# Performance work log

Hardware: AMD Instinct MI355X
Metric: run time of the kernel (lower is better)

## Reference

```python
import jax, jax.numpy as jnp
import numpy as np

D, H, T, K = 512, 8, 4, 64   # dim, n_heads, n_tasks, topk_n
HD = D // H
PRUNE, EPS = 1e-3, 1e-8


def _ln(x, g, b, eps=1e-5):
    m = jnp.mean(x, axis=-1, keepdims=True)
    v = jnp.mean((x - m) ** 2, axis=-1, keepdims=True)
    return (x - m) * jax.lax.rsqrt(v + eps) * g + b


def setup_inputs() -> dict:
    key = jax.random.key(0)
    ks = jax.random.split(key, 5)
    B, N = 16, 8192
    tokens = jax.random.normal(ks[0], (B, N, D), jnp.float32)
    key_padding_mask = jax.random.uniform(ks[1], (B, N)) < 0.1  # True marks padding
    q = jax.random.normal(ks[2], (1, T, D), jnp.float32) * 0.02
    in_proj_w = jax.random.normal(ks[3], (3 * D, D), jnp.float32) / np.sqrt(D).astype(np.float32)
    in_proj_b = jnp.zeros((3 * D,), jnp.float32)
    pre_g = jnp.ones((D,), jnp.float32)
    pre_b = jnp.zeros((D,), jnp.float32)
    q_g = jnp.ones((D,), jnp.float32)
    q_b = jnp.zeros((D,), jnp.float32)
    log_tau = jnp.asarray(np.log(0.3), jnp.float32)
    return dict(tokens=tokens, key_padding_mask=key_padding_mask, q=q,
                in_proj_w=in_proj_w, in_proj_b=in_proj_b,
                pre_g=pre_g, pre_b=pre_b, q_g=q_g, q_b=q_b, log_tau=log_tau)


def reference(tokens, key_padding_mask, q, in_proj_w, in_proj_b,
              pre_g, pre_b, q_g, q_b, log_tau):
    B, N, _ = tokens.shape
    kpm = key_padding_mask  # [B,N], True = pad

    normed = _ln(tokens, pre_g, pre_b)                       # [B,N,D]
    tau = jnp.clip(jnp.exp(log_tau), 0.1, 10.0)
    query = _ln(q, q_g, q_b) / tau                           # [1,T,D]

    wq, wk, wv = in_proj_w[:D], in_proj_w[D:2 * D], in_proj_w[2 * D:]
    bq, bk, bv = in_proj_b[:D], in_proj_b[D:2 * D], in_proj_b[2 * D:]

    qp = (query[0] @ wq.T + bq).reshape(T, H, HD)            # [T,H,hd]
    kp = (normed @ wk.T + bk).reshape(B, N, H, HD)           # [B,N,H,hd]

    scores = jnp.einsum('thd,bnhd->bhtn', qp, kp) / np.float32(np.sqrt(HD))
    scores = jnp.where(kpm[:, None, None, :], -jnp.inf, scores)
    attn = jax.nn.softmax(scores, axis=-1)                   # [B,H,T,N]

    alpha = attn.mean(axis=1)                                # [B,T,N]
    alpha = jnp.where(kpm[:, None, :], 0.0, alpha)
    alpha = alpha / jnp.maximum(alpha.sum(-1, keepdims=True), EPS)

    # prune below threshold, with argmax one-hot fallback if everything pruned
    a = jnp.where(alpha < PRUNE, 0.0, alpha)
    a = jnp.where(kpm[:, None, :], 0.0, a)
    s = a.sum(-1, keepdims=True)
    need_fallback = s <= EPS                                 # [B,T,1]
    base = jnp.where(kpm[:, None, :], -1.0, alpha)
    onehot = jax.nn.one_hot(jnp.argmax(base, axis=-1), N, dtype=a.dtype)  # [B,T,N]
    a = jnp.where(need_fallback, onehot, a)
    a = jnp.where(kpm[:, None, :], 0.0, a)
    alpha = a / jnp.maximum(a.sum(-1, keepdims=True), EPS)

    # pool source: tie_mha_v projection of normed inputs
    pool_source = normed @ wv.T + bv                         # [B,N,D]

    # top-k gather + renorm weighting
    topv, topi = jax.lax.top_k(alpha, K)                     # [B,T,K]
    selected = jnp.take_along_axis(pool_source[:, None, :, :], topi[..., None], axis=2)  # [B,T,K,D]
    w = topv / jnp.maximum(topv.sum(-1, keepdims=True), EPS)
    pooled = (w[..., None] * selected).sum(axis=2)           # [B,T,D]
    return pooled
```

## Files before the change

kernel.cpp:

```cpp
#include <hip/hip_runtime.h>
#include <math.h>

#define Dd   512
#define Hh   8
#define Tt   4
#define HDd  64
#define Bb   16
#define Nn   8192
#define HTc  32
#define KS   64
#define NTOK (Bb*Nn)
#define PRUNEc 0.001f
#define EPSc   1e-8f

#define WS_G2     0u
#define WS_C1     65536u
#define WS_C0     65664u
#define WS_M      65792u
#define WS_L      67840u
#define WS_TOPW   69888u
#define WS_TOPI   86272u
#define WS_FLAG   102656u
#define WS_MEAN   131072u
#define WS_INV    655360u
#define WS_MASK8  1179648u
#define WS_SCORES 2097152u

__global__ void tap_detect(const unsigned* mraw, int* flag){
  int tid = threadIdx.x;
  if (tid == 0) *flag = 0;
  __syncthreads();
  int f = 0;
  for (int i = tid; i < NTOK/4; i += 256){
    unsigned v = mraw[i];
    if (v == 0x3f800000u) f |= 2;
    else if (v & ~1u)     f |= 1;
  }
  if (f) atomicOr(flag, f);
}

__global__ void tap_mask(const void* mraw, const int* flag, unsigned char* m8){
  int i = blockIdx.x*256 + threadIdx.x;
  int fl = *flag;
  unsigned char m;
  if (fl & 2)      m = (((const float*)mraw)[i] != 0.0f);
  else if (fl & 1) m = (((const unsigned char*)mraw)[i] != 0);
  else             m = (((const int*)mraw)[i] != 0);
  m8[i] = m;
}

__global__ void tap_prep(const float* q, const float* ipw, const float* ipb,
                         const float* pre_g, const float* pre_b,
                         const float* q_g, const float* q_b, const float* log_tau,
                         float* G2, float* C1, float* C0){
  __shared__ float query[Tt][Dd];
  __shared__ float qps[HDd];
  __shared__ float red[256];
  int tid = threadIdx.x;
  int ht = blockIdx.x;
  int h = ht >> 2, t = ht & 3;
  float tau = expf(log_tau[0]);
  tau = fminf(fmaxf(tau, 0.1f), 10.0f);
  float itau = 1.0f / tau;
  int wv = tid >> 6, lane = tid & 63;
  {
    const float* qr = q + wv*Dd;
    float s = 0.f, ss = 0.f;
    for (int j = lane; j < Dd; j += 64){ float x = qr[j]; s += x; ss += x*x; }
    #pragma unroll
    for (int off = 32; off; off >>= 1){ s += __shfl_down(s, off); ss += __shfl_down(ss, off); }
    s = __shfl(s, 0); ss = __shfl(ss, 0);
    float mean = s * (1.f/Dd);
    float var  = ss * (1.f/Dd) - mean*mean;
    float inv  = rsqrtf(var + 1e-5f);
    for (int j = lane; j < Dd; j += 64){
      float x = qr[j];
      query[wv][j] = ((x - mean)*inv*q_g[j] + q_b[j]) * itau;
    }
  }
  __syncthreads();
  {
    int d = tid >> 2, sub = tid & 3;
    int i = h*HDd + d;
    const float* wrow = ipw + (size_t)i*Dd;
    float acc = 0.f;
    int j0 = sub*128;
    for (int j = 0; j < 128; ++j) acc += query[t][j0+j]*wrow[j0+j];
    red[tid] = acc;
    __syncthreads();
    if (sub == 0) qps[d] = red[tid]+red[tid+1]+red[tid+2]+red[tid+3] + ipb[i];
    __syncthreads();
  }
  float c1p = 0.f, c0p = 0.f;
  for (int jj = 0; jj < 2; ++jj){
    int j = tid + jj*256;
    float acc = 0.f;
    #pragma unroll 8
    for (int d = 0; d < HDd; ++d)
      acc += qps[d] * ipw[(size_t)(Dd + h*HDd + d)*Dd + j];
    float w2 = acc * 0.125f;
    float g2 = w2 * pre_g[j];
    G2[ht*Dd + j] = g2;
    c1p += g2;
    c0p += w2 * pre_b[j];
  }
  if (tid < HDd) c0p += qps[tid] * ipb[Dd + h*HDd + tid] * 0.125f;
  red[tid] = c1p; __syncthreads();
  for (int s = 128; s; s >>= 1){ if (tid < s) red[tid] += red[tid+s]; __syncthreads(); }
  if (tid == 0) C1[ht] = red[0];
  __syncthreads();
  red[tid] = c0p; __syncthreads();
  for (int s = 128; s; s >>= 1){ if (tid < s) red[tid] += red[tid+s]; __syncthreads(); }
  if (tid == 0) C0[ht] = red[0];
}

__global__ __launch_bounds__(256, 3) void tap_scores(
    const float* __restrict__ tokens, const float* __restrict__ G2,
    const float* __restrict__ C1, const float* __restrict__ C0,
    float* __restrict__ scores, float* __restrict__ meanw, float* __restrict__ invw){
  __shared__ float4 xt4[64*33];
  __shared__ float4 g2s4[32*33];
  __shared__ float smean[64], sinv[64];
  int tid = threadIdx.x;
  int tg = tid & 15, hp = tid >> 4;
  int ht0 = hp, ht1 = hp + 16;
  size_t t0 = (size_t)blockIdx.x * 64;
  const float4* tokv = (const float4*)tokens;
  const float4* G2v  = (const float4*)G2;
  int colL = tid & 31, rowBase = tid >> 5;
  float acc[4][2] = {{0.f,0.f},{0.f,0.f},{0.f,0.f},{0.f,0.f}};
  float ps[8] = {0,0,0,0,0,0,0,0}, pss[8] = {0,0,0,0,0,0,0,0};
  for (int c = 0; c < 4; ++c){
    #pragma unroll
    for (int i = 0; i < 8; ++i){
      int row = rowBase + 8*i;
      float4 v = tokv[(t0 + row)*128 + c*32 + colL];
      xt4[row*33 + colL] = v;
      ps[i]  += v.x + v.y + v.z + v.w;
      pss[i] += v.x*v.x + v.y*v.y + v.z*v.z + v.w*v.w;
    }
    #pragma unroll
    for (int i = 0; i < 4; ++i){
      int p = tid + 256*i;
      int row = p >> 5;
      g2s4[row*33 + colL] = G2v[row*128 + c*32 + colL];
    }
    __syncthreads();
    const float4* xb = xt4 + tg*33;
    #pragma unroll 8
    for (int j4 = 0; j4 < 32; ++j4){
      float4 g0 = g2s4[ht0*33 + j4];
      float4 g1 = g2s4[ht1*33 + j4];
      #pragma unroll
      for (int r = 0; r < 4; ++r){
        float4 x = xb[r*528 + j4];
        acc[r][0] += x.x*g0.x + x.y*g0.y + x.z*g0.z + x.w*g0.w;
        acc[r][1] += x.x*g1.x + x.y*g1.y + x.z*g1.z + x.w*g1.w;
      }
    }
    __syncthreads();
  }
  #pragma unroll
  for (int i = 0; i < 8; ++i){
    float s = ps[i], ss = pss[i];
    #pragma unroll
    for (int off = 16; off; off >>= 1){
      s  += __shfl_down(s,  off, 32);
      ss += __shfl_down(ss, off, 32);
    }
    if ((tid & 31) == 0){
      int row = rowBase + 8*i;
      float mean = s * (1.f/512.f);
      float var  = ss * (1.f/512.f) - mean*mean;
      float inv  = rsqrtf(var + 1e-5f);
      smean[row] = mean; sinv[row] = inv;
      meanw[t0 + row] = mean; invw[t0 + row] = inv;
    }
  }
  __syncthreads();
  float c10 = C1[ht0], c11 = C1[ht1], c00 = C0[ht0], c01 = C0[ht1];
  int b  = (int)(t0 >> 13);
  int n0 = (int)(t0 & 8191);
  float* s0p = scores + ((size_t)(b*HTc + ht0))*Nn + n0 + tg;
  float* s1p = scores + ((size_t)(b*HTc + ht1))*Nn + n0 + tg;
  #pragma unroll
  for (int r = 0; r < 4; ++r){
    int row = tg + 16*r;
    float mean = smean[row], inv = sinv[row];
    s0p[16*r] = inv*(acc[r][0] - mean*c10) + c00;
    s1p[16*r] = inv*(acc[r][1] - mean*c11) + c01;
  }
}

__global__ void tap_norm(const float* __restrict__ scores, const unsigned char* __restrict__ m8,
                         float* __restrict__ mrow, float* __restrict__ lrow){
  int R = blockIdx.x;
  int b = R >> 5;
  const float* srow = scores + (size_t)R*Nn;
  const unsigned char* mk = m8 + b*Nn;
  int tid = threadIdx.x;
  int wv = tid >> 6, lane = tid & 63;
  __shared__ float r4[4];
  float v[32];
  float mx = -1e30f;
  #pragma unroll
  for (int i = 0; i < 32; ++i){
    int n = tid + i*256;
    float s = srow[n];
    v[i] = mk[n] ? -1e30f : s;
    mx = fmaxf(mx, v[i]);
  }
  #pragma unroll
  for (int off = 32; off; off >>= 1) mx = fmaxf(mx, __shfl_down(mx, off));
  if (lane == 0) r4[wv] = mx;
  __syncthreads();
  mx = fmaxf(fmaxf(r4[0], r4[1]), fmaxf(r4[2], r4[3]));
  float se = 0.f;
  #pragma unroll
  for (int i = 0; i < 32; ++i) se += expf(v[i] - mx);
  #pragma unroll
  for (int off = 32; off; off >>= 1) se += __shfl_down(se, off);
  __syncthreads();
  if (lane == 0) r4[wv] = se;
  __syncthreads();
  if (tid == 0){ mrow[R] = mx; lrow[R] = r4[0]+r4[1]+r4[2]+r4[3]; }
}

__global__ void tap_alpha(const float* __restrict__ scores, const unsigned char* __restrict__ m8,
                          const float* __restrict__ mrow, const float* __restrict__ lrow,
                          float* __restrict__ topw, int* __restrict__ topi){
  __shared__ float av[Nn];
  __shared__ float lv[1024];
  __shared__ int   li[1024];
  __shared__ float rv[4]; __shared__ int ri[4]; __shared__ int rp[4];
  __shared__ int cnt; __shared__ int sArg;
  int bt = blockIdx.x;
  int b = bt >> 2, t = bt & 3;
  int tid = threadIdx.x;
  int wv = tid >> 6, lane = tid & 63;
  const unsigned char* mk = m8 + b*Nn;
  if (tid == 0) cnt = 0;
  float mh[Hh], il[Hh];
  const float* srows[Hh];
  #pragma unroll
  for (int h = 0; h < Hh; ++h){
    int R = b*HTc + h*Tt + t;
    mh[h] = mrow[R];
    il[h] = 1.0f / lrow[R];
    srows[h] = scores + (size_t)R*Nn;
  }
  float lsum = 0.f;
  float bvv = -2.f; int bii = 1<<30;
  for (int i = 0; i < 32; ++i){
    int n = tid + i*256;
    float a = 0.f;
    if (!mk[n]){
      #pragma unroll
      for (int h = 0; h < Hh; ++h) a += expf(srows[h][n] - mh[h]) * il[h];
      a *= 0.125f;
    }
    av[n] = a;
    lsum += a;
    float bb = mk[n] ? -1.f : a;
    if (bb > bvv || (bb == bvv && n < bii)){ bvv = bb; bii = n; }
  }
  #pragma unroll
  for (int off = 32; off; off >>= 1) lsum += __shfl_down(lsum, off);
  if (lane == 0) rv[wv] = lsum;
  __syncthreads();
  float Sall = rv[0]+rv[1]+rv[2]+rv[3];
  #pragma unroll
  for (int off = 32; off; off >>= 1){
    float ov = __shfl_down(bvv, off);
    int   oi = __shfl_down(bii, off);
    if (ov > bvv || (ov == bvv && oi < bii)){ bvv = ov; bii = oi; }
  }
  __syncthreads();
  if (lane == 0){ rv[wv] = bvv; ri[wv] = bii; }
  __syncthreads();
  if (tid == 0){
    float bv2 = rv[0]; int bi2 = ri[0];
    for (int w2 = 1; w2 < 4; ++w2)
      if (rv[w2] > bv2 || (rv[w2] == bv2 && ri[w2] < bi2)){ bv2 = rv[w2]; bi2 = ri[w2]; }
    sArg = bi2;
  }
  __syncthreads();
  float f1 = 1.0f / fmaxf(Sall, EPSc);
  for (int i = 0; i < 32; ++i){
    int n = tid + i*256;
    float x = av[n] * f1;
    if (x >= PRUNEc){
      int id = atomicAdd(&cnt, 1);
      if (id < 1024){ lv[id] = x; li[id] = n; }
    }
  }
  __syncthreads();
  int L = cnt;
  float* tw = topw + bt*KS;
  int*   ti = topi + bt*KS;
  if (L == 0){
    if (tid < KS){ tw[tid] = (tid == 0) ? 1.f : 0.f; ti[tid] = (tid == 0) ? sArg : 0; }
    return;
  }
  if (L <= KS){
    if (tid < KS){ tw[tid] = (tid < L) ? lv[tid] : 0.f; ti[tid] = (tid < L) ? li[tid] : 0; }
    return;
  }
  for (int k = 0; k < KS; ++k){
    float bv = -1.f; int bn = 1<<30; int bp = -1;
    for (int j = tid; j < L; j += 256){
      float x = lv[j]; int nn = li[j];
      if (x > bv || (x == bv && nn < bn)){ bv = x; bn = nn; bp = j; }
    }
    #pragma unroll
    for (int off = 32; off; off >>= 1){
      float ov = __shfl_down(bv, off);
      int   on = __shfl_down(bn, off);
      int   op = __shfl_down(bp, off);
      if (ov > bv || (ov == bv && on < bn)){ bv = ov; bn = on; bp = op; }
    }
    if (lane == 0){ rv[wv] = bv; ri[wv] = bn; rp[wv] = bp; }
    __syncthreads();
    if (tid == 0){
      float bb = rv[0]; int bj = ri[0]; int pp = rp[0];
      for (int w2 = 1; w2 < 4; ++w2)
        if (rv[w2] > bb || (rv[w2] == bb && ri[w2] < bj)){ bb = rv[w2]; bj = ri[w2]; pp = rp[w2]; }
      tw[k] = bb; ti[k] = bj;
      lv[pp] = -1.f;
    }
    __syncthreads();
  }
}

__global__ void tap_pool(const float* __restrict__ tokens, const float* __restrict__ ipw,
                         const float* __restrict__ ipb,
                         const float* __restrict__ pre_g, const float* __restrict__ pre_b,
                         const float* __restrict__ meanw, const float* __restrict__ invw,
                         const float* __restrict__ topw, const int* __restrict__ topi,
                         float* __restrict__ out){
  __shared__ float wk_[KS]; __shared__ int rk_[KS];
  __shared__ float coeff[KS];
  __shared__ __align__(16) float u[Dd];
  __shared__ float sW, sS;
  int bt = blockIdx.x;
  int b = bt >> 2;
  int tid = threadIdx.x;
  if (tid < KS){ wk_[tid] = topw[bt*KS + tid]; rk_[tid] = topi[bt*KS + tid]; }
  __syncthreads();
  if (tid < KS){
    float v = wk_[tid];
    #pragma unroll
    for (int off = 32; off; off >>= 1) v += __shfl_down(v, off);
    if (tid == 0) sW = v;
  }
  __syncthreads();
  float sumw = sW;
  float Winv = 1.0f / fmaxf(sumw, EPSc);
  float Wn   = sumw * Winv;
  if (tid < KS){
    int n = rk_[tid];
    float mk = meanw[(size_t)b*Nn + n];
    float ik = invw [(size_t)b*Nn + n];
    float wn = wk_[tid] * Winv;
    coeff[tid] = wn * ik;
    float sp = wn * mk * ik;
    #pragma unroll
    for (int off = 32; off; off >>= 1) sp += __shfl_down(sp, off);
    if (tid == 0) sS = sp;
  }
  __syncthreads();
  float Sv = sS;
  int d0 = tid, d1 = tid + 256;
  float acc0 = 0.f, acc1 = 0.f;
  #pragma unroll 4
  for (int k = 0; k < KS; ++k){
    float c = coeff[k];
    const float* xr = tokens + ((size_t)b*Nn + rk_[k])*Dd;
    acc0 = fmaf(c, xr[d0], acc0);
    acc1 = fmaf(c, xr[d1], acc1);
  }
  u[d0] = pre_g[d0]*(acc0 - Sv) + pre_b[d0]*Wn;
  u[d1] = pre_g[d1]*(acc1 - Sv) + pre_b[d1]*Wn;
  __syncthreads();
  const float4* u4 = (const float4*)u;
  const float4* w0 = (const float4*)(ipw + (size_t)(2*Dd + d0)*Dd);
  const float4* w1 = (const float4*)(ipw + (size_t)(2*Dd + d1)*Dd);
  float o0 = 0.f, o1 = 0.f;
  #pragma unroll 4
  for (int j4 = 0; j4 < 128; ++j4){
    float4 uu = u4[j4];
    float4 a = w0[j4], c = w1[j4];
    o0 += uu.x*a.x + uu.y*a.y + uu.z*a.z + uu.w*a.w;
    o1 += uu.x*c.x + uu.y*c.y + uu.z*c.z + uu.w*c.w;
  }
  out[bt*Dd + d0] = o0 + Wn*ipb[2*Dd + d0];
  out[bt*Dd + d1] = o1 + Wn*ipb[2*Dd + d1];
}

extern "C" void kernel_launch(void* const* d_in, const int* in_sizes, int n_in,
                              void* d_out, int out_size, void* d_ws, size_t ws_size,
                              hipStream_t stream){
  const float* tokens = (const float*)d_in[0];
  const void*  kpm    = d_in[1];
  const float* q      = (const float*)d_in[2];
  const float* ipw    = (const float*)d_in[3];
  const float* ipb    = (const float*)d_in[4];
  const float* pre_g  = (const float*)d_in[5];
  const float* pre_b  = (const float*)d_in[6];
  const float* q_g    = (const float*)d_in[7];
  const float* q_b    = (const float*)d_in[8];
  const float* ltau   = (const float*)d_in[9];
  char* ws = (char*)d_ws;
  float* G2    = (float*)(ws + WS_G2);
  float* C1    = (float*)(ws + WS_C1);
  float* C0    = (float*)(ws + WS_C0);
  float* mrow  = (float*)(ws + WS_M);
  float* lrow  = (float*)(ws + WS_L);
  float* topwv = (float*)(ws + WS_TOPW);
  int*   topiv = (int*)  (ws + WS_TOPI);
  int*   flag  = (int*)  (ws + WS_FLAG);
  float* meanw = (float*)(ws + WS_MEAN);
  float* invw  = (float*)(ws + WS_INV);
  unsigned char* m8 = (unsigned char*)(ws + WS_MASK8);
  float* scores = (float*)(ws + WS_SCORES);
  float* out = (float*)d_out;

  hipLaunchKernelGGL(tap_detect, dim3(1), dim3(256), 0, stream, (const unsigned*)kpm, flag);
  hipLaunchKernelGGL(tap_mask,   dim3(NTOK/256), dim3(256), 0, stream, kpm, flag, m8);
  hipLaunchKernelGGL(tap_prep,   dim3(HTc), dim3(256), 0, stream,
                     q, ipw, ipb, pre_g, pre_b, q_g, q_b, ltau, G2, C1, C0);
  hipLaunchKernelGGL(tap_scores, dim3(NTOK/64), dim3(256), 0, stream,
                     tokens, G2, C1, C0, scores, meanw, invw);
  hipLaunchKernelGGL(tap_norm,   dim3(Bb*HTc), dim3(256), 0, stream, scores, m8, mrow, lrow);
  hipLaunchKernelGGL(tap_alpha,  dim3(Bb*Tt), dim3(256), 0, stream,
                     scores, m8, mrow, lrow, topwv, topiv);
  hipLaunchKernelGGL(tap_pool,   dim3(Bb*Tt), dim3(256), 0, stream,
                     tokens, ipw, ipb, pre_g, pre_b, meanw, invw, topwv, topiv, out);
}
```

Before: 618.6 us.

## Retile score GEMV into 512-token blocks with register prefetch and swizzled LDS

```diff
diff --git a/kernel.cpp b/kernel.cpp
--- a/kernel.cpp
+++ b/kernel.cpp
@@ -114,62 +114,86 @@
   if (tid == 0) C0[ht] = red[0];
 }
 
-__global__ __launch_bounds__(256, 3) void tap_scores(
+__global__ __launch_bounds__(256, 1) void tap_scores(
     const float* __restrict__ tokens, const float* __restrict__ G2,
     const float* __restrict__ C1, const float* __restrict__ C0,
     float* __restrict__ scores, float* __restrict__ meanw, float* __restrict__ invw){
-  __shared__ float4 xt4[64*33];
-  __shared__ float4 g2s4[32*33];
-  __shared__ float smean[64], sinv[64];
-  int tid = threadIdx.x;
-  int tg = tid & 15, hp = tid >> 4;
-  int ht0 = hp, ht1 = hp + 16;
-  size_t t0 = (size_t)blockIdx.x * 64;
+  __shared__ float4 xt[512*8];
+  __shared__ float4 g2s[32*128];
+  __shared__ float smean[512], sinv[512];
+  int tid = threadIdx.x;
+  int tg = tid & 63, hg = tid >> 6;
+  int srow = tid >> 3, scol = tid & 7;
+  int colp = scol ^ (srow & 7);
+  size_t t0 = (size_t)blockIdx.x * 512;
   const float4* tokv = (const float4*)tokens;
   const float4* G2v  = (const float4*)G2;
-  int colL = tid & 31, rowBase = tid >> 5;
-  float acc[4][2] = {{0.f,0.f},{0.f,0.f},{0.f,0.f},{0.f,0.f}};
-  float ps[8] = {0,0,0,0,0,0,0,0}, pss[8] = {0,0,0,0,0,0,0,0};
-  for (int c = 0; c < 4; ++c){
-    #pragma unroll
-    for (int i = 0; i < 8; ++i){
-      int row = rowBase + 8*i;
-      float4 v = tokv[(t0 + row)*128 + c*32 + colL];
-      xt4[row*33 + colL] = v;
-      ps[i]  += v.x + v.y + v.z + v.w;
-      pss[i] += v.x*v.x + v.y*v.y + v.z*v.z + v.w*v.w;
-    }
-    #pragma unroll
-    for (int i = 0; i < 4; ++i){
-      int p = tid + 256*i;
-      int row = p >> 5;
-      g2s4[row*33 + colL] = G2v[row*128 + c*32 + colL];
-    }
-    __syncthreads();
-    const float4* xb = xt4 + tg*33;
-    #pragma unroll 8
-    for (int j4 = 0; j4 < 32; ++j4){
-      float4 g0 = g2s4[ht0*33 + j4];
-      float4 g1 = g2s4[ht1*33 + j4];
+  float acc[8][8];
+  #pragma unroll
+  for (int r = 0; r < 8; ++r)
+    #pragma unroll
+    for (int u = 0; u < 8; ++u) acc[r][u] = 0.f;
+  float ps[16], pss[16];
+  #pragma unroll
+  for (int i = 0; i < 16; ++i){ ps[i] = 0.f; pss[i] = 0.f; }
+  float4 pre[16];
+  #pragma unroll
+  for (int i = 0; i < 16; ++i)
+    pre[i] = tokv[(t0 + srow + 32*i)*128 + scol];
+  #pragma unroll
+  for (int i = 0; i < 16; ++i){
+    int p = tid + 256*i;
+    g2s[p] = G2v[p];
+  }
+  #pragma unroll
+  for (int i = 0; i < 16; ++i){
+    float4 v = pre[i];
+    xt[(srow + 32*i)*8 + colp] = v;
+    ps[i]  += v.x + v.y + v.z + v.w;
+    pss[i] += v.x*v.x + v.y*v.y + v.z*v.z + v.w*v.w;
+  }
+  __syncthreads();
+  for (int c = 0; c < 16; ++c){
+    if (c < 15){
       #pragma unroll
-      for (int r = 0; r < 4; ++r){
-        float4 x = xb[r*528 + j4];
-        acc[r][0] += x.x*g0.x + x.y*g0.y + x.z*g0.z + x.w*g0.w;
-        acc[r][1] += x.x*g1.x + x.y*g1.y + x.z*g1.z + x.w*g1.w;
+      for (int i = 0; i < 16; ++i)
+        pre[i] = tokv[(t0 + srow + 32*i)*128 + (c+1)*8 + scol];
+    }
+    #pragma unroll
+    for (int j4 = 0; j4 < 8; ++j4){
+      float4 g[8];
+      #pragma unroll
+      for (int u = 0; u < 8; ++u) g[u] = g2s[(hg + 4*u)*128 + c*8 + j4];
+      #pragma unroll
+      for (int r = 0; r < 8; ++r){
+        float4 x = xt[(tg + 64*r)*8 + (j4 ^ (tg & 7))];
+        #pragma unroll
+        for (int u = 0; u < 8; ++u)
+          acc[r][u] += x.x*g[u].x + x.y*g[u].y + x.z*g[u].z + x.w*g[u].w;
       }
     }
-    __syncthreads();
-  }
-  #pragma unroll
-  for (int i = 0; i < 8; ++i){
+    if (c < 15){
+      __syncthreads();
+      #pragma unroll
+      for (int i = 0; i < 16; ++i){
+        float4 v = pre[i];
+        xt[(srow + 32*i)*8 + colp] = v;
+        ps[i]  += v.x + v.y + v.z + v.w;
+        pss[i] += v.x*v.x + v.y*v.y + v.z*v.z + v.w*v.w;
+      }
+      __syncthreads();
+    }
+  }
+  #pragma unroll
+  for (int i = 0; i < 16; ++i){
     float s = ps[i], ss = pss[i];
     #pragma unroll
-    for (int off = 16; off; off >>= 1){
-      s  += __shfl_down(s,  off, 32);
-      ss += __shfl_down(ss, off, 32);
-    }
-    if ((tid & 31) == 0){
-      int row = rowBase + 8*i;
+    for (int off = 4; off; off >>= 1){
+      s  += __shfl_down(s,  off, 8);
+      ss += __shfl_down(ss, off, 8);
+    }
+    if (scol == 0){
+      int row = srow + 32*i;
       float mean = s * (1.f/512.f);
       float var  = ss * (1.f/512.f) - mean*mean;
       float inv  = rsqrtf(var + 1e-5f);
@@ -178,17 +202,20 @@
     }
   }
   __syncthreads();
-  float c10 = C1[ht0], c11 = C1[ht1], c00 = C0[ht0], c01 = C0[ht1];
+  float c1v[8], c0v[8];
+  #pragma unroll
+  for (int u = 0; u < 8; ++u){ c1v[u] = C1[hg + 4*u]; c0v[u] = C0[hg + 4*u]; }
   int b  = (int)(t0 >> 13);
   int n0 = (int)(t0 & 8191);
-  float* s0p = scores + ((size_t)(b*HTc + ht0))*Nn + n0 + tg;
-  float* s1p = scores + ((size_t)(b*HTc + ht1))*Nn + n0 + tg;
-  #pragma unroll
-  for (int r = 0; r < 4; ++r){
-    int row = tg + 16*r;
+  #pragma unroll
+  for (int r = 0; r < 8; ++r){
+    int row = tg + 64*r;
     float mean = smean[row], inv = sinv[row];
-    s0p[16*r] = inv*(acc[r][0] - mean*c10) + c00;
-    s1p[16*r] = inv*(acc[r][1] - mean*c11) + c01;
+    #pragma unroll
+    for (int u = 0; u < 8; ++u){
+      int ht = hg + 4*u;
+      scores[((size_t)(b*HTc + ht))*Nn + n0 + row] = inv*(acc[r][u] - mean*c1v[u]) + c0v[u];
+    }
   }
 }
 
@@ -429,7 +456,7 @@
   hipLaunchKernelGGL(tap_mask,   dim3(NTOK/256), dim3(256), 0, stream, kpm, flag, m8);
   hipLaunchKernelGGL(tap_prep,   dim3(HTc), dim3(256), 0, stream,
                      q, ipw, ipb, pre_g, pre_b, q_g, q_b, ltau, G2, C1, C0);
-  hipLaunchKernelGGL(tap_scores, dim3(NTOK/64), dim3(256), 0, stream,
+  hipLaunchKernelGGL(tap_scores, dim3(NTOK/512), dim3(256), 0, stream,
                      tokens, G2, C1, C0, scores, meanw, invw);
   hipLaunchKernelGGL(tap_norm,   dim3(Bb*HTc), dim3(256), 0, stream, scores, m8, mrow, lrow);
   hipLaunchKernelGGL(tap_alpha,  dim3(Bb*Tt), dim3(256), 0, stream,
```

Result: slower. 1.269 ms (+105.1%).
